# Kernel optimization log

Hardware: AMD Instinct MI355X
Metric: run time of the kernel (lower is better)

Reference implementation:

```python
import jax, jax.numpy as jnp
import numpy as np

D_MODEL = 1024
N_HEAD = 16
D_K = D_MODEL // N_HEAD


def setup_inputs() -> dict:
    key = jax.random.key(0)
    ks = jax.random.split(key, 11)
    B, S = 4, 2048
    s = 1.0 / np.sqrt(D_MODEL)
    return {
        "q": jax.random.normal(ks[0], (B, S, D_MODEL), jnp.float32),
        "k": jax.random.normal(ks[1], (B, S, D_MODEL), jnp.float32),
        "v": jax.random.normal(ks[2], (B, S, D_MODEL), jnp.float32),
        "w_q": jax.random.normal(ks[3], (D_MODEL, D_MODEL), jnp.float32) * s,
        "b_q": jnp.zeros((D_MODEL,), jnp.float32),
        "w_k": jax.random.normal(ks[4], (D_MODEL, D_MODEL), jnp.float32) * s,
        "b_k": jnp.zeros((D_MODEL,), jnp.float32),
        "w_v": jax.random.normal(ks[5], (D_MODEL, D_MODEL), jnp.float32) * s,
        "b_v": jnp.zeros((D_MODEL,), jnp.float32),
        "w_o": jax.random.normal(ks[6], (D_MODEL, D_MODEL), jnp.float32) * s,
        "b_o": jnp.zeros((D_MODEL,), jnp.float32),
    }


def reference(q, k, v, w_q, b_q, w_k, b_k, w_v, b_v, w_o, b_o):
    B, S, _ = q.shape
    # projections (torch Linear: x @ W^T + b)
    qp = q @ w_q.T + b_q
    kp = k @ w_k.T + b_k
    vp = v @ w_v.T + b_v
    # split heads -> [B, H, S, d_k]
    qh = qp.reshape(B, S, N_HEAD, D_K).transpose(0, 2, 1, 3)
    kh = kp.reshape(B, S, N_HEAD, D_K).transpose(0, 2, 1, 3)
    vh = vp.reshape(B, S, N_HEAD, D_K).transpose(0, 2, 1, 3)
    # scaled dot-product attention
    scores = jnp.einsum("bhqd,bhkd->bhqk", qh, kh) / jnp.sqrt(jnp.float32(D_K)).astype(qh.dtype)
    attn = jax.nn.softmax(scores, axis=-1)
    out = jnp.einsum("bhqk,bhkd->bhqd", attn, vh)
    # merge heads -> [B, S, d_model]
    out = out.transpose(0, 2, 1, 3).reshape(B, S, D_MODEL)
    return out @ w_o.T + b_o
```

## Files before the change

### kernel.cpp

```cpp
#include <hip/hip_runtime.h>
#include <hip/hip_bf16.h>
#include <stdint.h>

#define D_MODEL 1024
#define SEQ     2048
#define NBATCH  4
#define NHEAD   16
#define MROWS   (NBATCH*SEQ)

typedef __attribute__((ext_vector_type(8))) short short8;
typedef __attribute__((ext_vector_type(4))) float floatx4;
typedef __attribute__((ext_vector_type(2))) unsigned int uint2v;

#if __has_builtin(__builtin_amdgcn_exp2f)
#define EXP2(x) __builtin_amdgcn_exp2f(x)
#else
#define EXP2(x) exp2f(x)
#endif

__device__ __forceinline__ unsigned short f2bf(float f) {
  unsigned int x;
  __builtin_memcpy(&x, &f, 4);
  x += 0x7fffu + ((x >> 16) & 1u);
  return (unsigned short)(x >> 16);
}

__device__ __forceinline__ unsigned int pk2(float a, float b) {
  __hip_bfloat162 h = __float22bfloat162_rn(make_float2(a, b));
  unsigned int u;
  __builtin_memcpy(&u, &h, 4);
  return u;
}

__device__ __forceinline__ void gl_lds16(const unsigned short* g, unsigned short* l) {
  __builtin_amdgcn_global_load_lds(
      (const __attribute__((address_space(1))) unsigned int*)g,
      (__attribute__((address_space(3))) unsigned int*)l, 16, 0, 0);
}

__global__ __launch_bounds__(256)
void cvt_all(const float* __restrict__ q, const float* __restrict__ k,
             const float* __restrict__ v, const float* __restrict__ wq,
             const float* __restrict__ wk, const float* __restrict__ wv,
             const float* __restrict__ wo,
             unsigned short* __restrict__ dq, unsigned short* __restrict__ dk,
             unsigned short* __restrict__ dv, unsigned short* __restrict__ dwq,
             unsigned short* __restrict__ dwk, unsigned short* __restrict__ dwv,
             unsigned short* __restrict__ dwo) {
  const unsigned QV4 = (MROWS * D_MODEL) / 4u;
  const unsigned WV4 = (D_MODEL * D_MODEL) / 4u;
  const unsigned total = 3u * QV4 + 4u * WV4;
  for (unsigned i = blockIdx.x * 256u + threadIdx.x; i < total;
       i += gridDim.x * 256u) {
    const float* s;
    unsigned short* d;
    unsigned off;
    if (i < 3u * QV4) {
      const unsigned t = i >> 21;
      off = i & (QV4 - 1u);
      s = (t == 0) ? q : (t == 1) ? k : v;
      d = (t == 0) ? dq : (t == 1) ? dk : dv;
    } else {
      const unsigned j = i - 3u * QV4;
      const unsigned t = j >> 18;
      off = j & (WV4 - 1u);
      s = (t == 0) ? wq : (t == 1) ? wk : (t == 2) ? wv : wo;
      d = (t == 0) ? dwq : (t == 1) ? dwk : (t == 2) ? dwv : dwo;
    }
    const floatx4 f = *(const floatx4*)(s + (size_t)off * 4);
    uint2v u;
    u.x = pk2(f[0], f[1]);
    u.y = pk2(f[2], f[3]);
    *(uint2v*)(d + (size_t)off * 4) = u;
  }
}

template <int OMODE>
__device__ __forceinline__ void gemm_body(const unsigned short* __restrict__ A,
                                          const unsigned short* __restrict__ W,
                                          const float* __restrict__ bias,
                                          void* __restrict__ Y_,
                                          int M, int N, int K, float scale,
                                          unsigned short* As, unsigned short* Bs) {
  const int tid  = threadIdx.x;
  const int lane = tid & 63;
  const int w    = tid >> 6;
  const int rho  = lane & 15;
  const int quad = lane >> 4;
  const int ntile = N >> 7;
  const int cpx = gridDim.x >> 3;
  const int wg  = (blockIdx.x & 7) * cpx + (blockIdx.x >> 3);
  const int bx = wg % ntile;
  const int by = wg / ntile;
  const int tm = by << 7, tn = bx << 7;
  const int wrow = (w >> 1) << 6;
  const int wcol = (w & 1) << 6;

  const int lrow = lane >> 3;
  const int g    = ((lane & 7) - lrow) & 7;
  const unsigned short* gA = A + (size_t)(tm + w * 32 + lrow) * K + g * 8;
  const unsigned short* gB = W + (size_t)(tn + w * 32 + lrow) * K + g * 8;

  floatx4 acc[4][4] = {};

#define GSTAGE(buf, kk)                                                        \
  _Pragma("unroll") for (int c = 0; c < 4; c++) {                              \
    gl_lds16(gA + (size_t)c * 8 * K + (kk), &As[(buf)*8192 + (w*256 + c*64)*8]); \
    gl_lds16(gB + (size_t)c * 8 * K + (kk), &Bs[(buf)*8192 + (w*256 + c*64)*8]); \
  }

  GSTAGE(0, 0);
  __syncthreads();

  for (int kk = 0; kk < K; kk += 64) {
    const int cur = (kk >> 6) & 1;
    if (kk + 64 < K) { GSTAGE(cur ^ 1, kk + 64); }
    const unsigned short* as = &As[cur * 8192];
    const unsigned short* bs = &Bs[cur * 8192];
#pragma unroll
    for (int h = 0; h < 2; h++) {
      const int kp = (quad + rho + h * 4) & 7;
      short8 af[4], bf4[4];
#pragma unroll
      for (int i = 0; i < 4; i++)
        af[i] = *(const short8*)&as[(wrow + i * 16 + rho) * 64 + kp * 8];
#pragma unroll
      for (int j = 0; j < 4; j++)
        bf4[j] = *(const short8*)&bs[(wcol + j * 16 + rho) * 64 + kp * 8];
#pragma unroll
      for (int i = 0; i < 4; i++)
#pragma unroll
        for (int j = 0; j < 4; j++)
          acc[i][j] = __builtin_amdgcn_mfma_f32_16x16x32_bf16(af[i], bf4[j],
                                                              acc[i][j], 0, 0, 0);
    }
    __syncthreads();
  }
#undef GSTAGE

  float bj[4];
#pragma unroll
  for (int j = 0; j < 4; j++) bj[j] = bias[tn + wcol + j * 16 + rho];
#pragma unroll
  for (int i = 0; i < 4; i++) {
    const int grow = tm + wrow + i * 16 + (quad << 2);
#pragma unroll
    for (int j = 0; j < 4; j++) {
      const int gcol = tn + wcol + j * 16 + rho;
#pragma unroll
      for (int r = 0; r < 4; r++) {
        const float val = (acc[i][j][r] + bj[j]) * scale;
        if (OMODE == 1)
          ((float*)Y_)[(size_t)(grow + r) * N + gcol] = val;
        else
          ((unsigned short*)Y_)[(size_t)(grow + r) * N + gcol] = f2bf(val);
      }
    }
  }
}

template <int OMODE>
__global__ __launch_bounds__(256, 2)
void gemm_one(const unsigned short* __restrict__ A,
              const unsigned short* __restrict__ W,
              const float* __restrict__ bias, void* __restrict__ Y_,
              int M, int N, int K, float scale) {
  __shared__ __attribute__((aligned(16))) unsigned short As[2 * 128 * 64];
  __shared__ __attribute__((aligned(16))) unsigned short Bs[2 * 128 * 64];
  gemm_body<OMODE>(A, W, bias, Y_, M, N, K, scale, As, Bs);
}

__global__ __launch_bounds__(256, 2)
void gemm_qkv(const unsigned short* __restrict__ qb, const unsigned short* __restrict__ wqb,
              const float* __restrict__ bq, unsigned short* __restrict__ Qp,
              const unsigned short* __restrict__ kb, const unsigned short* __restrict__ wkb,
              const float* __restrict__ bk, unsigned short* __restrict__ Kp,
              const unsigned short* __restrict__ vb, const unsigned short* __restrict__ wvb,
              const float* __restrict__ bv, unsigned short* __restrict__ Vp,
              float qscale) {
  __shared__ __attribute__((aligned(16))) unsigned short As[2 * 128 * 64];
  __shared__ __attribute__((aligned(16))) unsigned short Bs[2 * 128 * 64];
  const int y = blockIdx.y;
  const unsigned short* A = (y == 0) ? qb : (y == 1) ? kb : vb;
  const unsigned short* W = (y == 0) ? wqb : (y == 1) ? wkb : wvb;
  const float* bias       = (y == 0) ? bq : (y == 1) ? bk : bv;
  unsigned short* Y       = (y == 0) ? Qp : (y == 1) ? Kp : Vp;
  const float scale = (y == 0) ? qscale : 1.0f;
  gemm_body<0>(A, W, bias, Y, MROWS, D_MODEL, D_MODEL, scale, As, Bs);
}

__device__ __forceinline__ void attn_step(const unsigned short* __restrict__ ks,
                                          const unsigned short* __restrict__ vt,
                                          const short8 (&aq)[4][2],
                                          float (&lsum)[4], floatx4 (&oacc)[4][4],
                                          int rho, int quad, int kp0, int kp1) {
  floatx4 sc[4][4];
  __builtin_amdgcn_s_setprio(1);
#pragma unroll
  for (int gk = 0; gk < 4; gk++) {
    const int key = gk*16 + rho;
    const short8 kf0 = *(const short8*)(ks + (key*8 + kp0)*8);
    const short8 kf1 = *(const short8*)(ks + (key*8 + kp1)*8);
#pragma unroll
    for (int u = 0; u < 4; u++) {
      floatx4 t = {0.f, 0.f, 0.f, 0.f};
      t = __builtin_amdgcn_mfma_f32_16x16x32_bf16(kf0, aq[u][0], t, 0, 0, 0);
      t = __builtin_amdgcn_mfma_f32_16x16x32_bf16(kf1, aq[u][1], t, 0, 0, 0);
      sc[u][gk] = t;
    }
  }
  __builtin_amdgcn_s_setprio(0);
  short8 pa0[4], pa1[4];
#pragma unroll
  for (int u = 0; u < 4; u++) {
    float E[4][4];
#pragma unroll
    for (int gk = 0; gk < 4; gk++)
#pragma unroll
      for (int r = 0; r < 4; r++) E[gk][r] = EXP2(sc[u][gk][r]);
    float s01 = 0.f, s23 = 0.f;
#pragma unroll
    for (int r = 0; r < 4; r++) { s01 += E[0][r] + E[1][r]; s23 += E[2][r] + E[3][r]; }
    lsum[u] += s01 + s23;
    union { short8 s; unsigned int w4[4]; } a0, a1;
    a0.w4[0] = pk2(E[0][0], E[0][1]); a0.w4[1] = pk2(E[0][2], E[0][3]);
    a0.w4[2] = pk2(E[1][0], E[1][1]); a0.w4[3] = pk2(E[1][2], E[1][3]);
    a1.w4[0] = pk2(E[2][0], E[2][1]); a1.w4[1] = pk2(E[2][2], E[2][3]);
    a1.w4[2] = pk2(E[3][0], E[3][1]); a1.w4[3] = pk2(E[3][2], E[3][3]);
    pa0[u] = a0.s; pa1[u] = a1.s;
  }
  short8 bv0[4], bv1[4];
#pragma unroll
  for (int c = 0; c < 4; c++) {
    bv0[c] = *(const short8*)&vt[(c*16 + rho)*72 + quad*8];
    bv1[c] = *(const short8*)&vt[(c*16 + rho)*72 + 32 + quad*8];
  }
  __builtin_amdgcn_s_setprio(1);
#pragma unroll
  for (int u = 0; u < 4; u++)
#pragma unroll
    for (int c = 0; c < 4; c++) {
      oacc[u][c] = __builtin_amdgcn_mfma_f32_16x16x32_bf16(pa0[u], bv0[c], oacc[u][c], 0, 0, 0);
      oacc[u][c] = __builtin_amdgcn_mfma_f32_16x16x32_bf16(pa1[u], bv1[c], oacc[u][c], 0, 0, 0);
    }
  __builtin_amdgcn_s_setprio(0);
}

__global__ __launch_bounds__(256, 2)
void attn_fused(const unsigned short* __restrict__ Qp,
                const unsigned short* __restrict__ Kp,
                const unsigned short* __restrict__ Vp,
                unsigned short* __restrict__ AO) {
  __shared__ unsigned short Ks[2][64*64];
  __shared__ unsigned short Vt[2][64*72];

  const int tid  = threadIdx.x;
  const int w    = tid >> 6;
  const int lane = tid & 63;
  const int rho  = lane & 15;
  const int quad = lane >> 4;

  const int qt = blockIdx.x >> 6;
  const int bh = blockIdx.x & 63;
  const int b  = bh >> 4;
  const int h  = bh & 15;
  const size_t base = (size_t)b*SEQ*D_MODEL + h*64;
  const unsigned short* Qb = Qp + base;
  const unsigned short* Kb = Kp + base;
  const unsigned short* Vb = Vp + base;

  const int q0 = qt*256 + w*64;

  short8 aq[4][2];
#pragma unroll
  for (int u = 0; u < 4; u++) {
    const unsigned short* qr = Qb + (size_t)(q0 + u*16 + rho)*D_MODEL + quad*8;
    aq[u][0] = *(const short8*)qr;
    aq[u][1] = *(const short8*)(qr + 32);
  }

  float lsum[4] = {};
  floatx4 oacc[4][4] = {};

  const int vkap = ((lane >> 2) & 3) * 8 + ((lane >> 4) & 1) * 4 + (lane & 3)
                 + (lane >> 5) * 32;

  const int s0 = w*64 + lane;
  const int k0key = s0 >> 3, k0g = ((s0 & 7) - k0key) & 7;
  const int s1 = 256 + w*64 + lane;
  const int k1key = s1 >> 3, k1g = ((s1 & 7) - k1key) & 7;

  const int kp0 = (quad + rho) & 7;
  const int kp1 = (kp0 + 4) & 7;

#define VLOAD(v0r, v1r, kbase)                                                 \
  { const unsigned short* vr = Vb + (size_t)((kbase) + lane)*D_MODEL + w*16;   \
    v0r = *(const short8*)vr; v1r = *(const short8*)(vr + 8); }
#define VWRITE(buf, v0r, v1r)                                                  \
  { unsigned short* dst = &Vt[buf][w*16*72 + vkap];                            \
    _Pragma("unroll") for (int e = 0; e < 8; e++) dst[e*72] = (unsigned short)v0r[e]; \
    _Pragma("unroll") for (int e = 0; e < 8; e++) dst[(8+e)*72] = (unsigned short)v1r[e]; }
#define KSTAGE(buf, kbase)                                                     \
  { gl_lds16(Kb + (size_t)((kbase) + k0key)*D_MODEL + k0g*8, &Ks[buf][(w*64)*8]);      \
    gl_lds16(Kb + (size_t)((kbase) + k1key)*D_MODEL + k1g*8, &Ks[buf][(256 + w*64)*8]); }

  short8 vA0, vA1, vB0, vB1;
  VLOAD(vA0, vA1, 0);
  KSTAGE(0, 0);

  for (int kb = 0; kb < SEQ; kb += 128) {
    VWRITE(0, vA0, vA1);
    __syncthreads();
    VLOAD(vB0, vB1, kb + 64);
    KSTAGE(1, kb + 64);
    attn_step(&Ks[0][0], &Vt[0][0], aq, lsum, oacc, rho, quad, kp0, kp1);

    VWRITE(1, vB0, vB1);
    __syncthreads();
    if (kb + 128 < SEQ) {
      VLOAD(vA0, vA1, kb + 128);
      KSTAGE(0, kb + 128);
    }
    attn_step(&Ks[1][0], &Vt[1][0], aq, lsum, oacc, rho, quad, kp0, kp1);
  }
#undef VLOAD
#undef VWRITE
#undef KSTAGE

#pragma unroll
  for (int u = 0; u < 4; u++) {
    lsum[u] += __shfl_xor(lsum[u], 16);
    lsum[u] += __shfl_xor(lsum[u], 32);
  }

#pragma unroll
  for (int u = 0; u < 4; u++) {
    float inv[4];
#pragma unroll
    for (int r = 0; r < 4; r++)
      inv[r] = 1.0f / __shfl(lsum[u], quad * 4 + r, 64);
#pragma unroll
    for (int c = 0; c < 4; c++)
#pragma unroll
      for (int r = 0; r < 4; r++)
        AO[base + (size_t)(q0 + u*16 + (quad << 2) + r)*D_MODEL + c*16 + rho] =
            f2bf(oacc[u][c][r] * inv[r]);
  }
}

extern "C" void kernel_launch(void* const* d_in, const int* in_sizes, int n_in,
                              void* d_out, int out_size, void* d_ws, size_t ws_size,
                              hipStream_t stream) {
  const float* q  = (const float*)d_in[0];
  const float* k  = (const float*)d_in[1];
  const float* v  = (const float*)d_in[2];
  const float* wq = (const float*)d_in[3];
  const float* bq = (const float*)d_in[4];
  const float* wk = (const float*)d_in[5];
  const float* bk = (const float*)d_in[6];
  const float* wv = (const float*)d_in[7];
  const float* bv = (const float*)d_in[8];
  const float* wo = (const float*)d_in[9];
  const float* bo = (const float*)d_in[10];
  float* out = (float*)d_out;

  unsigned short* Qp  = (unsigned short*)d_ws;
  unsigned short* Kp  = Qp + (size_t)MROWS*D_MODEL;
  unsigned short* Vp  = Kp + (size_t)MROWS*D_MODEL;
  unsigned short* AO  = Vp + (size_t)MROWS*D_MODEL;
  unsigned short* qb  = AO + (size_t)MROWS*D_MODEL;
  unsigned short* kb  = qb + (size_t)MROWS*D_MODEL;
  unsigned short* vb  = kb + (size_t)MROWS*D_MODEL;
  unsigned short* wqb = vb + (size_t)MROWS*D_MODEL;
  unsigned short* wkb = wqb + (size_t)D_MODEL*D_MODEL;
  unsigned short* wvb = wkb + (size_t)D_MODEL*D_MODEL;
  unsigned short* wob = wvb + (size_t)D_MODEL*D_MODEL;

  const float qscale = 0.125f * 1.4426950408889634f;

  const dim3 blk(256);
  cvt_all<<<dim3(2048), blk, 0, stream>>>(q, k, v, wq, wk, wv, wo,
                                          qb, kb, vb, wqb, wkb, wvb, wob);

  gemm_qkv<<<dim3((D_MODEL/128) * (MROWS/128), 3), blk, 0, stream>>>(
      qb, wqb, bq, Qp, kb, wkb, bk, Kp, vb, wvb, bv, Vp, qscale);

  attn_fused<<<dim3(NBATCH*NHEAD*(SEQ/256)), blk, 0, stream>>>(Qp, Kp, Vp, AO);

  gemm_one<1><<<dim3((D_MODEL/128) * (MROWS/128)), blk, 0, stream>>>(
      AO, wob, bo, out, MROWS, D_MODEL, D_MODEL, 1.0f);
}
```

Before: 321.5 us.

## Emit V projection pre-transposed and stage it into LDS asynchronously

The QKV projection GEMM now writes V in a per-head transposed layout, with keys permuted to match the MFMA operand order. The attention kernel can then stage V tiles with the same direct global-to-LDS loads used for K, instead of loading V into registers and scattering 2-byte transposed writes into LDS. This removes the scalar LDS scatter and register staging from the attention loop. In exchange, the GEMM epilogue for V does scattered 2-byte global stores with poor coalescing.

Measured after the change: 349.0 us. +8.5%, slower.

```diff
diff --git a/kernel.cpp b/kernel.cpp
--- a/kernel.cpp
+++ b/kernel.cpp
@@ -81,7 +81,8 @@
                                           const float* __restrict__ bias,
                                           void* __restrict__ Y_,
                                           int M, int N, int K, float scale,
-                                          unsigned short* As, unsigned short* Bs) {
+                                          unsigned short* As, unsigned short* Bs,
+                                          int vtrans) {
   const int tid  = threadIdx.x;
   const int lane = tid & 63;
   const int w    = tid >> 6;
@@ -150,10 +151,20 @@
 #pragma unroll
       for (int r = 0; r < 4; r++) {
         const float val = (acc[i][j][r] + bj[j]) * scale;
-        if (OMODE == 1)
+        if (OMODE == 1) {
           ((float*)Y_)[(size_t)(grow + r) * N + gcol] = val;
-        else
+        } else if (vtrans) {
+          const int gr  = grow + r;
+          const int bq_ = gr >> 11, sq = gr & 2047;
+          const int hh  = gcol >> 6, dd = gcol & 63;
+          const int k6  = sq & 63;
+          const int p   = ((k6 >> 2) & 3) * 8 + ((k6 >> 4) & 1) * 4
+                        + (k6 & 3) + (k6 >> 5) * 32;
+          ((unsigned short*)Y_)[(size_t)((bq_ * 16 + hh) * 64 + dd) * 2048 +
+                                (sq & ~63) + p] = f2bf(val);
+        } else {
           ((unsigned short*)Y_)[(size_t)(grow + r) * N + gcol] = f2bf(val);
+        }
       }
     }
   }
@@ -167,7 +178,7 @@
               int M, int N, int K, float scale) {
   __shared__ __attribute__((aligned(16))) unsigned short As[2 * 128 * 64];
   __shared__ __attribute__((aligned(16))) unsigned short Bs[2 * 128 * 64];
-  gemm_body<OMODE>(A, W, bias, Y_, M, N, K, scale, As, Bs);
+  gemm_body<OMODE>(A, W, bias, Y_, M, N, K, scale, As, Bs, 0);
 }
 
 __global__ __launch_bounds__(256, 2)
@@ -186,11 +197,12 @@
   const float* bias       = (y == 0) ? bq : (y == 1) ? bk : bv;
   unsigned short* Y       = (y == 0) ? Qp : (y == 1) ? Kp : Vp;
   const float scale = (y == 0) ? qscale : 1.0f;
-  gemm_body<0>(A, W, bias, Y, MROWS, D_MODEL, D_MODEL, scale, As, Bs);
+  gemm_body<0>(A, W, bias, Y, MROWS, D_MODEL, D_MODEL, scale, As, Bs,
+               (y == 2) ? 1 : 0);
 }
 
 __device__ __forceinline__ void attn_step(const unsigned short* __restrict__ ks,
-                                          const unsigned short* __restrict__ vt,
+                                          const unsigned short* __restrict__ vs,
                                           const short8 (&aq)[4][2],
                                           float (&lsum)[4], floatx4 (&oacc)[4][4],
                                           int rho, int quad, int kp0, int kp1) {
@@ -232,8 +244,8 @@
   short8 bv0[4], bv1[4];
 #pragma unroll
   for (int c = 0; c < 4; c++) {
-    bv0[c] = *(const short8*)&vt[(c*16 + rho)*72 + quad*8];
-    bv1[c] = *(const short8*)&vt[(c*16 + rho)*72 + 32 + quad*8];
+    bv0[c] = *(const short8*)&vs[(c*16 + rho)*64 + kp0*8];
+    bv1[c] = *(const short8*)&vs[(c*16 + rho)*64 + kp1*8];
   }
   __builtin_amdgcn_s_setprio(1);
 #pragma unroll
@@ -249,10 +261,10 @@
 __global__ __launch_bounds__(256, 2)
 void attn_fused(const unsigned short* __restrict__ Qp,
                 const unsigned short* __restrict__ Kp,
-                const unsigned short* __restrict__ Vp,
+                const unsigned short* __restrict__ VpT,
                 unsigned short* __restrict__ AO) {
   __shared__ unsigned short Ks[2][64*64];
-  __shared__ unsigned short Vt[2][64*72];
+  __shared__ unsigned short Vs[2][64*64];
 
   const int tid  = threadIdx.x;
   const int w    = tid >> 6;
@@ -267,7 +279,7 @@
   const size_t base = (size_t)b*SEQ*D_MODEL + h*64;
   const unsigned short* Qb = Qp + base;
   const unsigned short* Kb = Kp + base;
-  const unsigned short* Vb = Vp + base;
+  const unsigned short* VbT = VpT + (size_t)(b*16 + h) * 64 * 2048;
 
   const int q0 = qt*256 + w*64;
 
@@ -282,50 +294,42 @@
   float lsum[4] = {};
   floatx4 oacc[4][4] = {};
 
-  const int vkap = ((lane >> 2) & 3) * 8 + ((lane >> 4) & 1) * 4 + (lane & 3)
-                 + (lane >> 5) * 32;
-
   const int s0 = w*64 + lane;
   const int k0key = s0 >> 3, k0g = ((s0 & 7) - k0key) & 7;
   const int s1 = 256 + w*64 + lane;
   const int k1key = s1 >> 3, k1g = ((s1 & 7) - k1key) & 7;
 
+  const int vr0 = s0 >> 3, vg0 = ((s0 & 7) - vr0) & 7;
+  const int vr1 = s1 >> 3, vg1 = ((s1 & 7) - vr1) & 7;
+
   const int kp0 = (quad + rho) & 7;
   const int kp1 = (kp0 + 4) & 7;
 
-#define VLOAD(v0r, v1r, kbase)                                                 \
-  { const unsigned short* vr = Vb + (size_t)((kbase) + lane)*D_MODEL + w*16;   \
-    v0r = *(const short8*)vr; v1r = *(const short8*)(vr + 8); }
-#define VWRITE(buf, v0r, v1r)                                                  \
-  { unsigned short* dst = &Vt[buf][w*16*72 + vkap];                            \
-    _Pragma("unroll") for (int e = 0; e < 8; e++) dst[e*72] = (unsigned short)v0r[e]; \
-    _Pragma("unroll") for (int e = 0; e < 8; e++) dst[(8+e)*72] = (unsigned short)v1r[e]; }
 #define KSTAGE(buf, kbase)                                                     \
   { gl_lds16(Kb + (size_t)((kbase) + k0key)*D_MODEL + k0g*8, &Ks[buf][(w*64)*8]);      \
     gl_lds16(Kb + (size_t)((kbase) + k1key)*D_MODEL + k1g*8, &Ks[buf][(256 + w*64)*8]); }
-
-  short8 vA0, vA1, vB0, vB1;
-  VLOAD(vA0, vA1, 0);
+#define VSTAGE(buf, kbase)                                                     \
+  { gl_lds16(VbT + (size_t)vr0*2048 + (kbase) + vg0*8, &Vs[buf][(w*64)*8]);            \
+    gl_lds16(VbT + (size_t)vr1*2048 + (kbase) + vg1*8, &Vs[buf][(256 + w*64)*8]); }
+
   KSTAGE(0, 0);
+  VSTAGE(0, 0);
 
   for (int kb = 0; kb < SEQ; kb += 128) {
-    VWRITE(0, vA0, vA1);
     __syncthreads();
-    VLOAD(vB0, vB1, kb + 64);
     KSTAGE(1, kb + 64);
-    attn_step(&Ks[0][0], &Vt[0][0], aq, lsum, oacc, rho, quad, kp0, kp1);
-
-    VWRITE(1, vB0, vB1);
+    VSTAGE(1, kb + 64);
+    attn_step(&Ks[0][0], &Vs[0][0], aq, lsum, oacc, rho, quad, kp0, kp1);
+
     __syncthreads();
     if (kb + 128 < SEQ) {
-      VLOAD(vA0, vA1, kb + 128);
       KSTAGE(0, kb + 128);
-    }
-    attn_step(&Ks[1][0], &Vt[1][0], aq, lsum, oacc, rho, quad, kp0, kp1);
-  }
-#undef VLOAD
-#undef VWRITE
+      VSTAGE(0, kb + 128);
+    }
+    attn_step(&Ks[1][0], &Vs[1][0], aq, lsum, oacc, rho, quad, kp0, kp1);
+  }
 #undef KSTAGE
+#undef VSTAGE
 
 #pragma unroll
   for (int u = 0; u < 4; u++) {
```
